# Performance work log

Measured on AMD Instinct MI355X. Metric: run time of the kernel, lower is better.

The kernel has to match this reference:

```python
import jax, jax.numpy as jnp
import numpy as np

S = 60            # voxel grid side
N = 100000        # active voxels
M_PAD = 60000     # padded pairs per kernel offset
C_IN = 64
C_OUT = 64
KV = 27           # kernel volume (3^3)
CENTER = 13


def _build_maps():
    rng = np.random.default_rng(0)
    lin = rng.choice(S ** 3, size=N, replace=False)
    coords = np.stack(np.unravel_index(lin, (S, S, S)), axis=1).astype(np.int64)  # [N,3]
    lut = -np.ones(S ** 3, dtype=np.int64)
    lut[lin] = np.arange(N)
    imap = -np.ones((KV - 1, M_PAD), dtype=np.int32)
    omap = -np.ones((KV - 1, M_PAD), dtype=np.int32)
    row = 0
    for k in range(KV):
        if k == CENTER:
            continue
        d = np.array([k // 9 - 1, (k // 3) % 3 - 1, k % 3 - 1])
        nb = coords + d
        valid = np.all((nb >= 0) & (nb < S), axis=1)
        linnb = nb[:, 0] * S * S + nb[:, 1] * S + nb[:, 2]
        j = np.where(valid, lut[np.clip(linnb, 0, S ** 3 - 1)], -1)
        mask = j >= 0
        src = np.nonzero(mask)[0].astype(np.int32)   # input idx (gather)
        dst = j[mask].astype(np.int32)               # output idx (scatter)
        m = min(src.shape[0], M_PAD)
        imap[row, :m] = src[:m]
        omap[row, :m] = dst[:m]
        row += 1
    return imap, omap


def setup_inputs() -> dict:
    key = jax.random.key(0)
    kf, kw = jax.random.split(key)
    feats = jax.random.normal(kf, (N, C_IN), dtype=jnp.float32)
    stdv = 1.0 / np.sqrt(C_OUT * KV)
    kernel = jax.random.uniform(kw, (KV, C_IN, C_OUT), dtype=jnp.float32,
                                minval=-stdv, maxval=stdv)
    imap_np, omap_np = _build_maps()
    return {
        "feats": feats,
        "kernel": kernel,
        "imap": jnp.asarray(imap_np),
        "omap": jnp.asarray(omap_np),
    }


def reference(feats, kernel, imap, omap):
    # Submanifold sparse 3D conv: center weight applied densely,
    # 26 neighbor offsets via gather -> per-offset GEMM -> scatter-add.
    # feats: [N, Cin], kernel: [27, Cin, Cout], imap/omap: [26, M] (-1 = pad)
    koff = jnp.concatenate([jnp.arange(CENTER), jnp.arange(CENTER + 1, KV)])
    w_off = kernel[koff]                                   # [26, Cin, Cout]
    out = feats @ kernel[CENTER]                           # [N, Cout] center GEMM
    valid = (imap >= 0)                                    # [26, M]
    gathered = feats[jnp.clip(imap, 0)] * valid[..., None].astype(feats.dtype)  # [26, M, Cin]
    partial = jnp.einsum('kmc,kco->kmo', gathered, w_off)  # [26, M, Cout]
    dst = jnp.where(valid, omap, 0).reshape(-1)            # padded rows contribute zeros
    out = out.at[dst].add(partial.reshape(-1, partial.shape[-1]))
    return out
```

## Files before the change

kernel.cpp:

```cpp
#include <hip/hip_runtime.h>


#define N_PTS 100000
#define MPAD  60000
#define C     64
#define NSL   27

typedef short bf16x8 __attribute__((ext_vector_type(8)));
typedef float f32x4  __attribute__((ext_vector_type(4)));

static __device__ inline unsigned short f2bf(float x) {
    unsigned int u = __float_as_uint(x);
    u += 0x7fffu + ((u >> 16) & 1u);
    return (unsigned short)(u >> 16);
}

#define FEATS16_BYTES ((size_t)(N_PTS + 1) * C * 2)
#define WFRAG_OFF     (((FEATS16_BYTES) + 255) & ~(size_t)255)
#define WFRAG_BYTES   ((size_t)NSL * 8192)
#define NBR_OFF       (WFRAG_OFF + WFRAG_BYTES)
#define NBR_BYTES     ((size_t)26 * N_PTS * 4)

#define FEAT_ITEMS 800008
#define WF_ITEMS   (NSL * 2 * 4 * 64)
#define SCAT_ITEMS (26 * MPAD / 4)
#define PREP_TOTAL (FEAT_ITEMS + WF_ITEMS + SCAT_ITEMS)

__global__ __launch_bounds__(256) void prep_one(const float* __restrict__ feats,
                                                const float* __restrict__ kern,
                                                const int* __restrict__ imap,
                                                const int* __restrict__ omap,
                                                unsigned short* __restrict__ f16,
                                                unsigned short* __restrict__ wf,
                                                int* __restrict__ nbr) {
    const int idx = blockIdx.x * 256 + threadIdx.x;
    if (idx < FEAT_ITEMS) {
        bf16x8* dst = (bf16x8*)f16;
        if (idx < FEAT_ITEMS - 8) {
            const float4* src = (const float4*)feats;
            const float4 a = src[2 * idx];
            const float4 b = src[2 * idx + 1];
            bf16x8 v;
            v[0] = (short)f2bf(a.x); v[1] = (short)f2bf(a.y);
            v[2] = (short)f2bf(a.z); v[3] = (short)f2bf(a.w);
            v[4] = (short)f2bf(b.x); v[5] = (short)f2bf(b.y);
            v[6] = (short)f2bf(b.z); v[7] = (short)f2bf(b.w);
            dst[idx] = v;
        } else {
            dst[idx] = (bf16x8){0, 0, 0, 0, 0, 0, 0, 0};
        }
    } else if (idx < FEAT_ITEMS + WF_ITEMS) {
        const int w = idx - FEAT_ITEMS;
        const int lane = w & 63;
        const int rest = w >> 6;
        const int ct = rest & 3;
        const int kk = (rest >> 2) & 1;
        const int s  = rest >> 3;
        bf16x8 v = (bf16x8){0, 0, 0, 0, 0, 0, 0, 0};
        if (s < NSL) {
            const int q = lane >> 4, t = lane & 15;
            const int ksrc = (s == 26) ? 13 : (s + (s >= 13 ? 1 : 0));
            const int k0 = kk * 32 + q * 8;
            const int n  = ct * 16 + t;
            const float* wp = kern + (size_t)ksrc * 4096 + n;
            #pragma unroll
            for (int j = 0; j < 8; ++j) v[j] = (short)f2bf(wp[(size_t)(k0 + j) * 64]);
        }
        ((bf16x8*)wf)[w] = v;
    } else {
        const int k = idx - (FEAT_ITEMS + WF_ITEMS);
        if (k < SCAT_ITEMS) {
            const int s = k / (MPAD / 4);
            const int v = k - s * (MPAD / 4);
            const int4 iv = ((const int4*)(imap + (size_t)s * MPAD))[v];
            const int4 ov = ((const int4*)(omap + (size_t)s * MPAD))[v];
            int* nb = nbr + (size_t)s * N_PTS;
            if (iv.x >= 0) nb[ov.x] = iv.x;
            if (iv.y >= 0) nb[ov.y] = iv.y;
            if (iv.z >= 0) nb[ov.z] = iv.z;
            if (iv.w >= 0) nb[ov.w] = iv.w;
        }
    }
}

__global__ __launch_bounds__(128, 3) void spconv_main(const unsigned short* __restrict__ f16,
                                                      const unsigned short* __restrict__ wf,
                                                      const int* __restrict__ nbr,
                                                      float* __restrict__ out) {
    const int lane = threadIdx.x & 63;
    const int wave = threadIdx.x >> 6;
    const int q = lane >> 4, t = lane & 15;
    const int R0 = blockIdx.x * 64 + wave * 32;
    const int row0 = R0 + t;
    const int row1 = R0 + 16 + t;
    const bool inb0 = (row0 < N_PTS);
    const bool inb1 = (row1 < N_PTS);
    const int safe0 = inb0 ? row0 : 0;
    const int safe1 = inb1 ? row1 : 0;

    const bf16x8* fv = (const bf16x8*)f16;
    const bf16x8* bv = (const bf16x8*)wf;

    int j0r[26], j1r[26];
    #pragma unroll
    for (int s = 0; s < 26; ++s) {
        j0r[s] = nbr[(size_t)s * N_PTS + safe0];
        j1r[s] = nbr[(size_t)s * N_PTS + safe1];
    }

    f32x4 acc[2][4];
    #pragma unroll
    for (int a = 0; a < 2; ++a)
        #pragma unroll
        for (int c = 0; c < 4; ++c)
            acc[a][c] = (f32x4){0.f, 0.f, 0.f, 0.f};

    #pragma unroll
    for (int s = 0; s < NSL; ++s) {
        int j0, j1;
        if (s == 26) {
            j0 = inb0 ? row0 : -1;
            j1 = inb1 ? row1 : -1;
        } else {
            j0 = inb0 ? j0r[s] : -1;
            j1 = inb1 ? j1r[s] : -1;
        }
        const int jz0 = ((unsigned)j0 < (unsigned)N_PTS) ? j0 : N_PTS;
        const int jz1 = ((unsigned)j1 < (unsigned)N_PTS) ? j1 : N_PTS;
        const bf16x8* a0p = fv + (size_t)jz0 * 8;
        const bf16x8* a1p = fv + (size_t)jz1 * 8;
        const bf16x8 A0 = a0p[q];
        const bf16x8 A1 = a0p[4 + q];
        const bf16x8 A2 = a1p[q];
        const bf16x8 A3 = a1p[4 + q];
        const bf16x8* bp = bv + (size_t)s * 512;
        bf16x8 B0[4], B1[4];
        #pragma unroll
        for (int ct = 0; ct < 4; ++ct) {
            B0[ct] = bp[ct * 64 + lane];
            B1[ct] = bp[256 + ct * 64 + lane];
        }
        #pragma unroll
        for (int ct = 0; ct < 4; ++ct) {
            acc[0][ct] = __builtin_amdgcn_mfma_f32_16x16x32_bf16(A0, B0[ct], acc[0][ct], 0, 0, 0);
            acc[1][ct] = __builtin_amdgcn_mfma_f32_16x16x32_bf16(A2, B0[ct], acc[1][ct], 0, 0, 0);
        }
        #pragma unroll
        for (int ct = 0; ct < 4; ++ct) {
            acc[0][ct] = __builtin_amdgcn_mfma_f32_16x16x32_bf16(A1, B1[ct], acc[0][ct], 0, 0, 0);
            acc[1][ct] = __builtin_amdgcn_mfma_f32_16x16x32_bf16(A3, B1[ct], acc[1][ct], 0, 0, 0);
        }
    }

    #pragma unroll
    for (int tile = 0; tile < 2; ++tile) {
        #pragma unroll
        for (int i = 0; i < 4; ++i) {
            const int r = R0 + tile * 16 + 4 * q + i;
            if (r < N_PTS) {
                #pragma unroll
                for (int ct = 0; ct < 4; ++ct)
                    out[(size_t)r * C + ct * 16 + t] = acc[tile][ct][i];
            }
        }
    }
}

extern "C" void kernel_launch(void* const* d_in, const int* in_sizes, int n_in,
                              void* d_out, int out_size, void* d_ws, size_t ws_size,
                              hipStream_t stream) {
    const float* feats = (const float*)d_in[0];
    const float* kern  = (const float*)d_in[1];
    const int*   imap  = (const int*)d_in[2];
    const int*   omap  = (const int*)d_in[3];

    char* ws = (char*)d_ws;
    unsigned short* f16 = (unsigned short*)ws;
    unsigned short* wfr = (unsigned short*)(ws + WFRAG_OFF);
    int*            nbr = (int*)(ws + NBR_OFF);

    prep_one<<<dim3((PREP_TOTAL + 255) / 256), dim3(256), 0, stream>>>(
        feats, kern, imap, omap, f16, wfr, nbr);
    spconv_main<<<dim3((N_PTS + 63) / 64), dim3(128), 0, stream>>>(
        f16, wfr, nbr, (float*)d_out);
}
```

Baseline: 158.4 us.

## Software-pipeline neighbor gathers through LDS with async global_load_lds triple buffering

Replaces the upfront load of all 26 neighbor indices into registers and the per-offset direct global gathers with a software pipeline. Feature rows are gathered asynchronously into a per-wave triple-buffered LDS region via global_load_lds two offsets ahead, while indices and weight fragments are prefetched into double-buffered registers. Explicit vmcnt waits and s_setprio around the MFMA block aim to overlap gather latency with matrix math and cut register pressure. The cost is hand-tuned wait counts that depend on instruction ordering, which risks correctness if the compiler reorders loads, plus 24KB of LDS per block that may limit occupancy.

```diff
diff --git a/kernel.cpp b/kernel.cpp
--- a/kernel.cpp
+++ b/kernel.cpp
@@ -87,6 +87,8 @@
                                                       const unsigned short* __restrict__ wf,
                                                       const int* __restrict__ nbr,
                                                       float* __restrict__ out) {
+    __shared__ __align__(16) char smem[2][3][4096];
+
     const int lane = threadIdx.x & 63;
     const int wave = threadIdx.x >> 6;
     const int q = lane >> 4, t = lane & 15;
@@ -100,13 +102,48 @@
 
     const bf16x8* fv = (const bf16x8*)f16;
     const bf16x8* bv = (const bf16x8*)wf;
-
-    int j0r[26], j1r[26];
-    #pragma unroll
-    for (int s = 0; s < 26; ++s) {
-        j0r[s] = nbr[(size_t)s * N_PTS + safe0];
-        j1r[s] = nbr[(size_t)s * N_PTS + safe1];
-    }
+    char* abuf = (char*)smem[wave];
+
+    int jr0[2], jr1[2];
+    bf16x8 Br[2][8];
+
+#define LOADJ(s) do { \
+        jr0[(s) & 1] = nbr[(size_t)(s) * N_PTS + safe0]; \
+        jr1[(s) & 1] = nbr[(size_t)(s) * N_PTS + safe1]; \
+    } while (0)
+
+#define GATHER(s) do { \
+        int j0, j1; \
+        if ((s) == 26) { j0 = inb0 ? row0 : -1; j1 = inb1 ? row1 : -1; } \
+        else           { j0 = inb0 ? jr0[(s) & 1] : -1; j1 = inb1 ? jr1[(s) & 1] : -1; } \
+        const int jz0 = ((unsigned)j0 < (unsigned)N_PTS) ? j0 : N_PTS; \
+        const int jz1 = ((unsigned)j1 < (unsigned)N_PTS) ? j1 : N_PTS; \
+        const char* g0 = (const char*)(fv + (size_t)jz0 * 8) + q * 16; \
+        const char* g1 = (const char*)(fv + (size_t)jz1 * 8) + q * 16; \
+        char* db = abuf + ((s) % 3) * 4096; \
+        __builtin_amdgcn_global_load_lds((const __attribute__((address_space(1))) unsigned int*)(g0), \
+            (__attribute__((address_space(3))) unsigned int*)(db), 16, 0, 0); \
+        __builtin_amdgcn_global_load_lds((const __attribute__((address_space(1))) unsigned int*)(g0 + 64), \
+            (__attribute__((address_space(3))) unsigned int*)(db + 1024), 16, 0, 0); \
+        __builtin_amdgcn_global_load_lds((const __attribute__((address_space(1))) unsigned int*)(g1), \
+            (__attribute__((address_space(3))) unsigned int*)(db + 2048), 16, 0, 0); \
+        __builtin_amdgcn_global_load_lds((const __attribute__((address_space(1))) unsigned int*)(g1 + 64), \
+            (__attribute__((address_space(3))) unsigned int*)(db + 3072), 16, 0, 0); \
+    } while (0)
+
+#define LOADB(s) do { \
+        const bf16x8* bp = bv + (size_t)(s) * 512; \
+        _Pragma("unroll") \
+        for (int ct = 0; ct < 4; ++ct) { \
+            Br[(s) & 1][ct]     = bp[ct * 64 + lane]; \
+            Br[(s) & 1][4 + ct] = bp[256 + ct * 64 + lane]; \
+        } \
+    } while (0)
+
+    LOADJ(0); LOADJ(1);
+    GATHER(0); GATHER(1);
+    LOADJ(2);
+    LOADB(0);
 
     f32x4 acc[2][4];
     #pragma unroll
@@ -117,40 +154,36 @@
 
     #pragma unroll
     for (int s = 0; s < NSL; ++s) {
-        int j0, j1;
-        if (s == 26) {
-            j0 = inb0 ? row0 : -1;
-            j1 = inb1 ? row1 : -1;
-        } else {
-            j0 = inb0 ? j0r[s] : -1;
-            j1 = inb1 ? j1r[s] : -1;
-        }
-        const int jz0 = ((unsigned)j0 < (unsigned)N_PTS) ? j0 : N_PTS;
-        const int jz1 = ((unsigned)j1 < (unsigned)N_PTS) ? j1 : N_PTS;
-        const bf16x8* a0p = fv + (size_t)jz0 * 8;
-        const bf16x8* a1p = fv + (size_t)jz1 * 8;
-        const bf16x8 A0 = a0p[q];
-        const bf16x8 A1 = a0p[4 + q];
-        const bf16x8 A2 = a1p[q];
-        const bf16x8 A3 = a1p[4 + q];
-        const bf16x8* bp = bv + (size_t)s * 512;
-        bf16x8 B0[4], B1[4];
+        if (s + 2 <= 26) GATHER(s + 2);
+        if (s + 3 <= 25) LOADJ(s + 3);
+        if (s + 1 <= 26) LOADB(s + 1);
+
+        if (s <= 24) asm volatile("s_waitcnt vmcnt(14)" ::: "memory");
+        else         asm volatile("s_waitcnt vmcnt(8)"  ::: "memory");
+
+        const char* db = abuf + (s % 3) * 4096;
+        const bf16x8 A0 = *(const bf16x8*)(db +    0 + lane * 16);
+        const bf16x8 A1 = *(const bf16x8*)(db + 1024 + lane * 16);
+        const bf16x8 A2 = *(const bf16x8*)(db + 2048 + lane * 16);
+        const bf16x8 A3 = *(const bf16x8*)(db + 3072 + lane * 16);
+
+        __builtin_amdgcn_s_setprio(1);
         #pragma unroll
         for (int ct = 0; ct < 4; ++ct) {
-            B0[ct] = bp[ct * 64 + lane];
-            B1[ct] = bp[256 + ct * 64 + lane];
+            acc[0][ct] = __builtin_amdgcn_mfma_f32_16x16x32_bf16(A0, Br[s & 1][ct], acc[0][ct], 0, 0, 0);
+            acc[1][ct] = __builtin_amdgcn_mfma_f32_16x16x32_bf16(A2, Br[s & 1][ct], acc[1][ct], 0, 0, 0);
         }
         #pragma unroll
         for (int ct = 0; ct < 4; ++ct) {
-            acc[0][ct] = __builtin_amdgcn_mfma_f32_16x16x32_bf16(A0, B0[ct], acc[0][ct], 0, 0, 0);
-            acc[1][ct] = __builtin_amdgcn_mfma_f32_16x16x32_bf16(A2, B0[ct], acc[1][ct], 0, 0, 0);
-        }
-        #pragma unroll
-        for (int ct = 0; ct < 4; ++ct) {
-            acc[0][ct] = __builtin_amdgcn_mfma_f32_16x16x32_bf16(A1, B1[ct], acc[0][ct], 0, 0, 0);
-            acc[1][ct] = __builtin_amdgcn_mfma_f32_16x16x32_bf16(A3, B1[ct], acc[1][ct], 0, 0, 0);
-        }
+            acc[0][ct] = __builtin_amdgcn_mfma_f32_16x16x32_bf16(A1, Br[s & 1][4 + ct], acc[0][ct], 0, 0, 0);
+            acc[1][ct] = __builtin_amdgcn_mfma_f32_16x16x32_bf16(A3, Br[s & 1][4 + ct], acc[1][ct], 0, 0, 0);
+        }
+        __builtin_amdgcn_s_setprio(0);
     }
+
+#undef LOADJ
+#undef GATHER
+#undef LOADB
 
     #pragma unroll
     for (int tile = 0; tile < 2; ++tile) {
```

New measurement: 155.9 us. About the same (-1.6%).

## Double-buffer gathered features and weights in LDS via async global-to-LDS loads

Applied to the files above, without the earlier changes.

Restructures the main loop into a software pipeline: the next offset's weight slice and gathered feature rows are fetched straight into LDS with global_load_lds while the current offset's MFMAs run. Weights are shared across four waves per block (block size doubled to 256), and neighbor indices are loaded two offsets ahead instead of all 26 up front. This cuts register pressure and hides gather latency, at the cost of manual vmcnt bookkeeping, per-offset barriers and extra LDS traffic.

```diff
diff --git a/kernel.cpp b/kernel.cpp
--- a/kernel.cpp
+++ b/kernel.cpp
@@ -83,14 +83,25 @@
     }
 }
 
-__global__ __launch_bounds__(128, 3) void spconv_main(const unsigned short* __restrict__ f16,
+static __device__ inline void gl_lds(const char* g, char* l) {
+    __builtin_amdgcn_global_load_lds(
+        (const __attribute__((address_space(1))) unsigned int*)g,
+        (__attribute__((address_space(3))) unsigned int*)l, 16, 0, 0);
+}
+
+#define WAITV(n) asm volatile("s_waitcnt vmcnt(" #n ")" ::: "memory")
+
+__global__ __launch_bounds__(256, 3) void spconv_main(const unsigned short* __restrict__ f16,
                                                       const unsigned short* __restrict__ wf,
                                                       const int* __restrict__ nbr,
                                                       float* __restrict__ out) {
+    __shared__ __align__(16) char bsm[2][8192];
+    __shared__ __align__(16) char apool[4][2][4096];
+
     const int lane = threadIdx.x & 63;
     const int wave = threadIdx.x >> 6;
     const int q = lane >> 4, t = lane & 15;
-    const int R0 = blockIdx.x * 64 + wave * 32;
+    const int R0 = blockIdx.x * 128 + wave * 32;
     const int row0 = R0 + t;
     const int row1 = R0 + 16 + t;
     const bool inb0 = (row0 < N_PTS);
@@ -99,14 +110,43 @@
     const int safe1 = inb1 ? row1 : 0;
 
     const bf16x8* fv = (const bf16x8*)f16;
-    const bf16x8* bv = (const bf16x8*)wf;
-
-    int j0r[26], j1r[26];
-    #pragma unroll
-    for (int s = 0; s < 26; ++s) {
-        j0r[s] = nbr[(size_t)s * N_PTS + safe0];
-        j1r[s] = nbr[(size_t)s * N_PTS + safe1];
-    }
+    const char* wfb  = (const char*)wf;
+    char* arng = (char*)apool[wave];
+
+    int jr0[2], jr1[2];
+
+#define LOADJ(s_) do { \
+        jr0[(s_) & 1] = nbr[(size_t)(s_) * N_PTS + safe0]; \
+        jr1[(s_) & 1] = nbr[(size_t)(s_) * N_PTS + safe1]; \
+    } while (0)
+
+#define GATHER(s_) do { \
+        int j0, j1; \
+        if ((s_) == 26) { j0 = inb0 ? row0 : -1; j1 = inb1 ? row1 : -1; } \
+        else            { j0 = inb0 ? jr0[(s_) & 1] : -1; j1 = inb1 ? jr1[(s_) & 1] : -1; } \
+        const int jz0 = ((unsigned)j0 < (unsigned)N_PTS) ? j0 : N_PTS; \
+        const int jz1 = ((unsigned)j1 < (unsigned)N_PTS) ? j1 : N_PTS; \
+        const char* g0 = (const char*)(fv + (size_t)jz0 * 8) + q * 16; \
+        const char* g1 = (const char*)(fv + (size_t)jz1 * 8) + q * 16; \
+        char* db = arng + ((s_) & 1) * 4096; \
+        gl_lds(g0,      db);        \
+        gl_lds(g0 + 64, db + 1024); \
+        gl_lds(g1,      db + 2048); \
+        gl_lds(g1 + 64, db + 3072); \
+    } while (0)
+
+#define STAGEB(s_) do { \
+        const char* gs = wfb + (size_t)(s_) * 8192 + (size_t)(wave * 2) * 1024 + lane * 16; \
+        char* bd = bsm[(s_) & 1] + (wave * 2) * 1024; \
+        gl_lds(gs,        bd);        \
+        gl_lds(gs + 1024, bd + 1024); \
+    } while (0)
+
+    LOADJ(0); LOADJ(1);
+    STAGEB(0);
+    GATHER(0);
+    WAITV(4);
+    __builtin_amdgcn_s_barrier();
 
     f32x4 acc[2][4];
     #pragma unroll
@@ -116,30 +156,29 @@
             acc[a][c] = (f32x4){0.f, 0.f, 0.f, 0.f};
 
     #pragma unroll
-    for (int s = 0; s < NSL; ++s) {
-        int j0, j1;
-        if (s == 26) {
-            j0 = inb0 ? row0 : -1;
-            j1 = inb1 ? row1 : -1;
-        } else {
-            j0 = inb0 ? j0r[s] : -1;
-            j1 = inb1 ? j1r[s] : -1;
-        }
-        const int jz0 = ((unsigned)j0 < (unsigned)N_PTS) ? j0 : N_PTS;
-        const int jz1 = ((unsigned)j1 < (unsigned)N_PTS) ? j1 : N_PTS;
-        const bf16x8* a0p = fv + (size_t)jz0 * 8;
-        const bf16x8* a1p = fv + (size_t)jz1 * 8;
-        const bf16x8 A0 = a0p[q];
-        const bf16x8 A1 = a0p[4 + q];
-        const bf16x8 A2 = a1p[q];
-        const bf16x8 A3 = a1p[4 + q];
-        const bf16x8* bp = bv + (size_t)s * 512;
+    for (int st = 0; st < NSL; ++st) {
+        if (st + 1 < NSL) STAGEB(st + 1);
+        if (st + 2 < NSL - 1) LOADJ(st + 2);
+        if (st + 1 < NSL) GATHER(st + 1);
+
+        if (st <= 23)      WAITV(8);
+        else if (st <= 25) WAITV(6);
+        else               WAITV(0);
+
+        const char* ab = arng + (st & 1) * 4096;
+        const bf16x8 A0 = *(const bf16x8*)(ab +    0 + lane * 16);
+        const bf16x8 A1 = *(const bf16x8*)(ab + 1024 + lane * 16);
+        const bf16x8 A2 = *(const bf16x8*)(ab + 2048 + lane * 16);
+        const bf16x8 A3 = *(const bf16x8*)(ab + 3072 + lane * 16);
+        const char* bb = bsm[st & 1];
         bf16x8 B0[4], B1[4];
         #pragma unroll
         for (int ct = 0; ct < 4; ++ct) {
-            B0[ct] = bp[ct * 64 + lane];
-            B1[ct] = bp[256 + ct * 64 + lane];
-        }
+            B0[ct] = *(const bf16x8*)(bb +        ct * 1024 + lane * 16);
+            B1[ct] = *(const bf16x8*)(bb + 4096 + ct * 1024 + lane * 16);
+        }
+
+        __builtin_amdgcn_s_setprio(1);
         #pragma unroll
         for (int ct = 0; ct < 4; ++ct) {
             acc[0][ct] = __builtin_amdgcn_mfma_f32_16x16x32_bf16(A0, B0[ct], acc[0][ct], 0, 0, 0);
@@ -150,7 +189,15 @@
             acc[0][ct] = __builtin_amdgcn_mfma_f32_16x16x32_bf16(A1, B1[ct], acc[0][ct], 0, 0, 0);
             acc[1][ct] = __builtin_amdgcn_mfma_f32_16x16x32_bf16(A3, B1[ct], acc[1][ct], 0, 0, 0);
         }
+        __builtin_amdgcn_s_setprio(0);
+
+        if (st <= 23)      { WAITV(6); __builtin_amdgcn_s_barrier(); }
+        else if (st <= 25) { WAITV(4); __builtin_amdgcn_s_barrier(); }
     }
+
+#undef LOADJ
+#undef GATHER
+#undef STAGEB
 
     #pragma unroll
     for (int tile = 0; tile < 2; ++tile) {
@@ -181,6 +228,6 @@
 
     prep_one<<<dim3((PREP_TOTAL + 255) / 256), dim3(256), 0, stream>>>(
         feats, kern, imap, omap, f16, wfr, nbr);
-    spconv_main<<<dim3((N_PTS + 63) / 64), dim3(128), 0, stream>>>(
+    spconv_main<<<dim3((N_PTS + 127) / 128), dim3(256), 0, stream>>>(
         f16, wfr, nbr, (float*)d_out);
 }
```

Result: no change. 156.2 us (-1.4%).

## Software-pipeline neighbor gathers into LDS with async global_load_lds, one wave per block

Applied to the files above, without the earlier changes.

Restructures the main kernel so each single-wave block handles 64 rows with 16 accumulator tiles. Neighbor feature rows are gathered asynchronously into a triple-buffered LDS ring with global_load_lds, while the neighbor indices and weight fragments are prefetched into double-buffered registers a few offsets ahead. Hand-counted vmcnt waits and MFMA priority bumps are meant to overlap the irregular gather latency with matrix math. The risks are fewer waves per CU, since there are now 64-thread blocks with 24KB of LDS each, and fragile waitcnt counts that depend on how the compiler emits the loads.

```diff
diff --git a/kernel.cpp b/kernel.cpp
--- a/kernel.cpp
+++ b/kernel.cpp
@@ -83,77 +83,122 @@
     }
 }
 
-__global__ __launch_bounds__(128, 3) void spconv_main(const unsigned short* __restrict__ f16,
-                                                      const unsigned short* __restrict__ wf,
-                                                      const int* __restrict__ nbr,
-                                                      float* __restrict__ out) {
+static __device__ inline void gl_lds(const char* g, char* l) {
+    __builtin_amdgcn_global_load_lds(
+        (const __attribute__((address_space(1))) unsigned int*)g,
+        (__attribute__((address_space(3))) unsigned int*)l, 16, 0, 0);
+}
+
+#define WAITV(n) asm volatile("s_waitcnt vmcnt(" #n ")" ::: "memory")
+
+__global__ __launch_bounds__(64, 2) void spconv_main(const unsigned short* __restrict__ f16,
+                                                     const unsigned short* __restrict__ wf,
+                                                     const int* __restrict__ nbr,
+                                                     float* __restrict__ out) {
+    __shared__ __align__(16) char abuf[3][8192];
+
     const int lane = threadIdx.x & 63;
-    const int wave = threadIdx.x >> 6;
     const int q = lane >> 4, t = lane & 15;
-    const int R0 = blockIdx.x * 64 + wave * 32;
-    const int row0 = R0 + t;
-    const int row1 = R0 + 16 + t;
-    const bool inb0 = (row0 < N_PTS);
-    const bool inb1 = (row1 < N_PTS);
-    const int safe0 = inb0 ? row0 : 0;
-    const int safe1 = inb1 ? row1 : 0;
+    const int R0 = blockIdx.x * 64;
+    int rowi[4], safei[4];
+    bool inbi[4];
+    #pragma unroll
+    for (int i = 0; i < 4; ++i) {
+        rowi[i] = R0 + i * 16 + t;
+        inbi[i] = (rowi[i] < N_PTS);
+        safei[i] = inbi[i] ? rowi[i] : 0;
+    }
 
     const bf16x8* fv = (const bf16x8*)f16;
     const bf16x8* bv = (const bf16x8*)wf;
 
-    int j0r[26], j1r[26];
-    #pragma unroll
-    for (int s = 0; s < 26; ++s) {
-        j0r[s] = nbr[(size_t)s * N_PTS + safe0];
-        j1r[s] = nbr[(size_t)s * N_PTS + safe1];
-    }
-
-    f32x4 acc[2][4];
-    #pragma unroll
-    for (int a = 0; a < 2; ++a)
+    int jr[2][4];
+    bf16x8 Br[2][8];
+
+#define LOADJ(s_) do { \
+        _Pragma("unroll") \
+        for (int i = 0; i < 4; ++i) \
+            jr[(s_) & 1][i] = nbr[(size_t)(s_) * N_PTS + safei[i]]; \
+    } while (0)
+
+#define GATHER(s_) do { \
+        char* db = (char*)abuf[(s_) % 3]; \
+        _Pragma("unroll") \
+        for (int i = 0; i < 4; ++i) { \
+            int j_; \
+            if ((s_) == 26) j_ = inbi[i] ? rowi[i] : -1; \
+            else            j_ = inbi[i] ? jr[(s_) & 1][i] : -1; \
+            const int jz = ((unsigned)j_ < (unsigned)N_PTS) ? j_ : N_PTS; \
+            const char* g = (const char*)(fv + (size_t)jz * 8) + q * 16; \
+            gl_lds(g,      db + (i * 2 + 0) * 1024); \
+            gl_lds(g + 64, db + (i * 2 + 1) * 1024); \
+        } \
+    } while (0)
+
+#define LOADB(s_) do { \
+        const bf16x8* bp = bv + (size_t)(s_) * 512; \
+        _Pragma("unroll") \
+        for (int ct = 0; ct < 4; ++ct) { \
+            Br[(s_) & 1][ct]     = bp[ct * 64 + lane]; \
+            Br[(s_) & 1][4 + ct] = bp[256 + ct * 64 + lane]; \
+        } \
+    } while (0)
+
+    LOADJ(0);
+    GATHER(0);
+    LOADJ(1);
+    LOADB(0);
+    GATHER(1);
+    LOADJ(2);
+
+    f32x4 acc[4][4];
+    #pragma unroll
+    for (int a = 0; a < 4; ++a)
         #pragma unroll
         for (int c = 0; c < 4; ++c)
             acc[a][c] = (f32x4){0.f, 0.f, 0.f, 0.f};
 
     #pragma unroll
     for (int s = 0; s < NSL; ++s) {
-        int j0, j1;
-        if (s == 26) {
-            j0 = inb0 ? row0 : -1;
-            j1 = inb1 ? row1 : -1;
-        } else {
-            j0 = inb0 ? j0r[s] : -1;
-            j1 = inb1 ? j1r[s] : -1;
-        }
-        const int jz0 = ((unsigned)j0 < (unsigned)N_PTS) ? j0 : N_PTS;
-        const int jz1 = ((unsigned)j1 < (unsigned)N_PTS) ? j1 : N_PTS;
-        const bf16x8* a0p = fv + (size_t)jz0 * 8;
-        const bf16x8* a1p = fv + (size_t)jz1 * 8;
-        const bf16x8 A0 = a0p[q];
-        const bf16x8 A1 = a0p[4 + q];
-        const bf16x8 A2 = a1p[q];
-        const bf16x8 A3 = a1p[4 + q];
-        const bf16x8* bp = bv + (size_t)s * 512;
-        bf16x8 B0[4], B1[4];
-        #pragma unroll
-        for (int ct = 0; ct < 4; ++ct) {
-            B0[ct] = bp[ct * 64 + lane];
-            B1[ct] = bp[256 + ct * 64 + lane];
-        }
-        #pragma unroll
-        for (int ct = 0; ct < 4; ++ct) {
-            acc[0][ct] = __builtin_amdgcn_mfma_f32_16x16x32_bf16(A0, B0[ct], acc[0][ct], 0, 0, 0);
-            acc[1][ct] = __builtin_amdgcn_mfma_f32_16x16x32_bf16(A2, B0[ct], acc[1][ct], 0, 0, 0);
-        }
-        #pragma unroll
-        for (int ct = 0; ct < 4; ++ct) {
-            acc[0][ct] = __builtin_amdgcn_mfma_f32_16x16x32_bf16(A1, B1[ct], acc[0][ct], 0, 0, 0);
-            acc[1][ct] = __builtin_amdgcn_mfma_f32_16x16x32_bf16(A3, B1[ct], acc[1][ct], 0, 0, 0);
-        }
-    }
-
-    #pragma unroll
-    for (int tile = 0; tile < 2; ++tile) {
+        if (s + 1 < NSL) LOADB(s + 1);
+        if (s + 2 < NSL) GATHER(s + 2);
+        if (s + 3 < NSL - 1) LOADJ(s + 3);
+
+        if (s <= 22)      WAITV(44);
+        else if (s == 23) WAITV(40);
+        else if (s == 24) WAITV(36);
+        else if (s == 25) WAITV(24);
+        else              WAITV(8);
+
+        const char* ab = (const char*)abuf[s % 3];
+        bf16x8 A[4][2];
+        #pragma unroll
+        for (int i = 0; i < 4; ++i) {
+            A[i][0] = *(const bf16x8*)(ab + (i * 2 + 0) * 1024 + lane * 16);
+            A[i][1] = *(const bf16x8*)(ab + (i * 2 + 1) * 1024 + lane * 16);
+        }
+        __builtin_amdgcn_s_setprio(1);
+        #pragma unroll
+        for (int i = 0; i < 4; ++i) {
+            #pragma unroll
+            for (int ct = 0; ct < 4; ++ct)
+                acc[i][ct] = __builtin_amdgcn_mfma_f32_16x16x32_bf16(A[i][0], Br[s & 1][ct], acc[i][ct], 0, 0, 0);
+        }
+        #pragma unroll
+        for (int i = 0; i < 4; ++i) {
+            #pragma unroll
+            for (int ct = 0; ct < 4; ++ct)
+                acc[i][ct] = __builtin_amdgcn_mfma_f32_16x16x32_bf16(A[i][1], Br[s & 1][4 + ct], acc[i][ct], 0, 0, 0);
+        }
+        __builtin_amdgcn_s_setprio(0);
+    }
+
+#undef LOADJ
+#undef GATHER
+#undef LOADB
+
+    #pragma unroll
+    for (int tile = 0; tile < 4; ++tile) {
         #pragma unroll
         for (int i = 0; i < 4; ++i) {
             const int r = R0 + tile * 16 + 4 * q + i;
@@ -181,6 +226,6 @@
 
     prep_one<<<dim3((PREP_TOTAL + 255) / 256), dim3(256), 0, stream>>>(
         feats, kern, imap, omap, f16, wfr, nbr);
-    spconv_main<<<dim3((N_PTS + 63) / 64), dim3(128), 0, stream>>>(
+    spconv_main<<<dim3((N_PTS + 63) / 64), dim3(64), 0, stream>>>(
         f16, wfr, nbr, (float*)d_out);
 }
```

Result: faster. 154.7 us (-2.3%).
